# Optimization experiments

Hardware: AMD Instinct MI355X
Metric: run time of the kernel (lower is better)

The kernel has to match this reference:

```python
import jax, jax.numpy as jnp
import numpy as np

D_MODEL = 128
NUM_HEADS = 4
HEAD_DIM = D_MODEL // NUM_HEADS  # 32
SCALE = 1.0 / np.sqrt(HEAD_DIM)
LAMBDA_INIT = 0.8
EPS = 1e-5


def _layernorm(x, w, b):
    mu = jnp.mean(x, axis=-1, keepdims=True)
    var = jnp.var(x, axis=-1, keepdims=True)
    return (x - mu) * jax.lax.rsqrt(var + EPS) * w + b


def setup_inputs() -> dict:
    key = jax.random.key(0)
    ks = jax.random.split(key, 10)
    B, T, D = 8, 2048, D_MODEL
    inp = {
        "tokens": jax.random.normal(ks[0], (B, T, D), dtype=jnp.float32),
        "ln_w": jnp.ones((D,), jnp.float32),
        "ln_b": jnp.zeros((D,), jnp.float32),
        "wq": jax.random.normal(ks[1], (D, 2 * D), jnp.float32) * (1.0 / np.sqrt(D)),
        "wk": jax.random.normal(ks[2], (D, 2 * D), jnp.float32) * (1.0 / np.sqrt(D)),
        "wv": jax.random.normal(ks[3], (D, 2 * D), jnp.float32) * (1.0 / np.sqrt(D)),
        "wo": jax.random.normal(ks[4], (2 * D, D), jnp.float32) * (1.0 / np.sqrt(2 * D)),
        "lambda_q1": jax.random.normal(ks[5], (HEAD_DIM,), jnp.float32) * 0.1,
        "lambda_k1": jax.random.normal(ks[6], (HEAD_DIM,), jnp.float32) * 0.1,
        "lambda_q2": jax.random.normal(ks[7], (HEAD_DIM,), jnp.float32) * 0.1,
        "lambda_k2": jax.random.normal(ks[8], (HEAD_DIM,), jnp.float32) * 0.1,
        "sigma_signal": jnp.asarray(3.0, jnp.float32),
        "sigma_noise": jnp.asarray(10.0, jnp.float32),
        "hn_w": jnp.ones((2 * HEAD_DIM,), jnp.float32),
        "hn_b": jnp.zeros((2 * HEAD_DIM,), jnp.float32),
    }
    return inp


def reference(tokens, ln_w, ln_b, wq, wk, wv, wo,
              lambda_q1, lambda_k1, lambda_q2, lambda_k2,
              sigma_signal, sigma_noise, hn_w, hn_b):
    B, T, D = tokens.shape
    H, hd = NUM_HEADS, HEAD_DIM

    x = _layernorm(tokens, ln_w, ln_b)

    def heads(x, w):  # [B,T,D] @ [D,2D] -> [B,H,T,2*hd]
        return (x @ w).reshape(B, T, H, 2 * hd).transpose(0, 2, 1, 3)

    q = heads(x, wq)
    k = heads(x, wk)
    v = heads(x, wv)
    q1, q2 = q[..., :hd], q[..., hd:]
    k1, k2 = k[..., :hd], k[..., hd:]

    scores1 = jnp.einsum('bhqd,bhkd->bhqk', q1, k1) * SCALE
    scores2 = jnp.einsum('bhqd,bhkd->bhqk', q2, k2) * SCALE

    # temporal Gaussian bias, shared sigma mode: [T,T] broadcast over [B,H]
    pos = jnp.arange(T, dtype=tokens.dtype)
    rel = pos[None, :] - pos[:, None]  # rel_dist[i,j] = j - i
    sig_s = jnp.maximum(sigma_signal, 1.0)
    sig_n = jnp.maximum(sigma_noise, 1.0)
    scores1 = scores1 + (-0.5 * (rel / sig_s) ** 2)
    scores2 = scores2 + (-0.5 * (rel / sig_n) ** 2)

    attn1 = jax.nn.softmax(scores1, axis=-1)
    attn2 = jax.nn.softmax(scores2, axis=-1)

    lam = jnp.exp(jnp.dot(lambda_q1, lambda_k1)) - jnp.exp(jnp.dot(lambda_q2, lambda_k2)) + LAMBDA_INIT

    out = jnp.einsum('bhqk,bhkd->bhqd', attn1 - lam * attn2, v)  # [B,H,T,2*hd]
    out = _layernorm(out, hn_w, hn_b)
    out = out * (1.0 - LAMBDA_INIT)
    out = out.transpose(0, 2, 1, 3).reshape(B, T, 2 * D)
    out = out @ wo
    return tokens + out
```

## Files before the change

### kernel.cpp

```cpp
#include <hip/hip_runtime.h>
#include <hip/hip_bf16.h>

#define TSEQ 2048
#define BATCH 8
#define NHEAD 4
#define BH (BATCH*NHEAD)
#define HD 32
#define SCALE 0.17677669529663687f
#define L2E   1.4426950408889634f
#define SCALE2 (SCALE * L2E)
#define LAMBDA_INIT 0.8f
#define LN_EPS 1e-5f

#if __has_builtin(__builtin_amdgcn_exp2f)
#define EXP2F(x) __builtin_amdgcn_exp2f(x)
#else
#define EXP2F(x) __expf((x) * 0.6931471805599453f)
#endif

typedef __attribute__((ext_vector_type(8))) short short8;
typedef __attribute__((ext_vector_type(4))) float f32x4;

static __device__ __forceinline__ unsigned short f2bf(float x) {
    union { __hip_bfloat16 h; unsigned short u; } cv;
    cv.h = __float2bfloat16(x);
    return cv.u;
}

__global__ __launch_bounds__(256) void k_prep(
    const float* __restrict__ wq, const float* __restrict__ wk,
    const float* __restrict__ wv, const float* __restrict__ wo,
    const float* __restrict__ lq1, const float* __restrict__ lk1,
    const float* __restrict__ lq2, const float* __restrict__ lk2,
    const float* __restrict__ sig_s_p, const float* __restrict__ sig_n_p,
    unsigned short* __restrict__ WqkvT, unsigned short* __restrict__ WoT,
    float* __restrict__ scal)
{
    __shared__ float xt[64][65];
    const int bid = blockIdx.x, tid = threadIdx.x;

    if (bid == 0 && tid == 0) {
        float d1 = 0.f, d2 = 0.f;
        for (int i = 0; i < HD; i++) { d1 += lq1[i] * lk1[i]; d2 += lq2[i] * lk2[i]; }
        float lam = __expf(d1) - __expf(d2) + LAMBDA_INIT;
        float ss = fmaxf(sig_s_p[0], 1.f);
        float sn = fmaxf(sig_n_p[0], 1.f);
        int W = (int)ceilf(fmaxf(ss, sn) * 6.f);
        W = (W + 31) & ~31;
        if (W < 64) W = 64;
        scal[0] = lam;
        scal[1] = -0.5f / (ss * ss) * L2E;
        scal[2] = -0.5f / (sn * sn) * L2E;
        scal[3] = (float)W;
    }

    const float* src; int srcN, k0, nsrc0, dstK;
    unsigned short* dst;
    if (bid < 24) {
        int ntile = bid >> 1, ktile = bid & 1;
        int gn0 = ntile * 64; k0 = ktile * 64;
        int mat = gn0 >> 8;
        src = (mat == 0) ? wq : (mat == 1 ? wk : wv);
        srcN = 256; nsrc0 = gn0 & 255;
        dst = WqkvT + (size_t)gn0 * 128; dstK = 128;
    } else {
        int b2 = bid - 24;
        int ntile = b2 >> 2, ktile = b2 & 3;
        int gn0 = ntile * 64; k0 = ktile * 64;
        src = wo; srcN = 128; nsrc0 = gn0;
        dst = WoT + (size_t)gn0 * 256; dstK = 256;
    }
    {
        int r = tid >> 2, cs = tid & 3;
        const float* sp = src + (size_t)(k0 + r) * srcN + nsrc0 + cs * 16;
        #pragma unroll
        for (int j = 0; j < 4; j++) {
            float4 v = *(const float4*)(sp + j * 4);
            xt[r][cs * 16 + j * 4 + 0] = v.x;
            xt[r][cs * 16 + j * 4 + 1] = v.y;
            xt[r][cs * 16 + j * 4 + 2] = v.z;
            xt[r][cs * 16 + j * 4 + 3] = v.w;
        }
    }
    __syncthreads();
    {
        int n = tid >> 2, ks = tid & 3;
        short8 o0, o1;
        #pragma unroll
        for (int j = 0; j < 8; j++) {
            o0[j] = (short)f2bf(xt[ks * 16 + j][n]);
            o1[j] = (short)f2bf(xt[ks * 16 + 8 + j][n]);
        }
        unsigned short* dp = dst + (size_t)n * dstK + k0 + ks * 16;
        *(short8*)dp = o0;
        *(short8*)(dp + 8) = o1;
    }
}

__global__ __launch_bounds__(256) void k_qkv(
    const float* __restrict__ tokens, const float* __restrict__ ln_w,
    const float* __restrict__ ln_b, const unsigned short* __restrict__ WqkvT,
    unsigned short* __restrict__ Qg, unsigned short* __restrict__ Kg,
    unsigned short* __restrict__ Vtg)
{
    __shared__ unsigned short x_lds[32][132];
    __shared__ unsigned short c_lds[4][16][68];
    const int tid = threadIdx.x;
    const int r0 = blockIdx.x * 32;

    {
        int row = tid >> 3, sub = tid & 7;
        const float* tr = tokens + (size_t)(r0 + row) * 128 + sub * 16;
        float v[16]; float s = 0.f, sq = 0.f;
        #pragma unroll
        for (int j = 0; j < 16; j += 4) {
            float4 t4 = *(const float4*)(tr + j);
            v[j] = t4.x; v[j + 1] = t4.y; v[j + 2] = t4.z; v[j + 3] = t4.w;
        }
        #pragma unroll
        for (int j = 0; j < 16; j++) { s += v[j]; sq += v[j] * v[j]; }
        #pragma unroll
        for (int m = 1; m < 8; m <<= 1) { s += __shfl_xor(s, m, 64); sq += __shfl_xor(sq, m, 64); }
        float mean = s * (1.f / 128.f);
        float var  = sq * (1.f / 128.f) - mean * mean;
        float rstd = rsqrtf(var + LN_EPS);
        short8 o0, o1;
        #pragma unroll
        for (int j = 0; j < 8; j++) {
            int c0 = sub * 16 + j, c1 = sub * 16 + 8 + j;
            o0[j] = (short)f2bf((v[j] - mean) * rstd * ln_w[c0] + ln_b[c0]);
            o1[j] = (short)f2bf((v[8 + j] - mean) * rstd * ln_w[c1] + ln_b[c1]);
        }
        *(short8*)&x_lds[row][sub * 16] = o0;
        *(short8*)&x_lds[row][sub * 16 + 8] = o1;
    }
    __syncthreads();

    const int w = tid >> 6, lane = tid & 63;
    const int lg = lane >> 4, li = lane & 15;
    const int rt = w >> 1, ch = w & 1;

    short8 a[4];
    #pragma unroll
    for (int kc = 0; kc < 4; kc++)
        a[kc] = *(const short8*)&x_lds[rt * 16 + li][kc * 32 + lg * 8];

    const int b   = r0 >> 11;
    const int tw0 = (r0 & 2047) + rt * 16;

    #pragma unroll
    for (int cc = 0; cc < 6; cc++) {
        f32x4 acc[4] = {};
        #pragma unroll
        for (int t = 0; t < 4; t++) {
            int n0 = ch * 384 + cc * 64 + t * 16;
            const unsigned short* bp = WqkvT + (size_t)(n0 + li) * 128 + lg * 8;
            #pragma unroll
            for (int kc = 0; kc < 4; kc++) {
                short8 bf = *(const short8*)(bp + kc * 32);
                acc[t] = __builtin_amdgcn_mfma_f32_16x16x32_bf16(a[kc], bf, acc[t], 0, 0, 0);
            }
        }
        #pragma unroll
        for (int t = 0; t < 4; t++)
            #pragma unroll
            for (int r = 0; r < 4; r++)
                c_lds[w][lg * 4 + r][t * 16 + li] = f2bf(acc[t][r]);

        int gc = ch * 6 + cc;
        int kind = gc >> 2, h = gc & 3;
        size_t bhh = (size_t)(b * NHEAD + h);
        if (kind < 2) {
            unsigned short* base = (kind == 0) ? Qg : Kg;
            int row = lane >> 2, seg = lane & 3;
            unsigned short* dp = base + (bhh * TSEQ + tw0 + row) * 64 + seg * 16;
            *(short8*)dp       = *(const short8*)&c_lds[w][row][seg * 16];
            *(short8*)(dp + 8) = *(const short8*)&c_lds[w][row][seg * 16 + 8];
        } else {
            int d = lane;
            short8 v0, v1;
            #pragma unroll
            for (int j = 0; j < 8; j++) {
                v0[j] = (short)c_lds[w][j][d];
                v1[j] = (short)c_lds[w][8 + j][d];
            }
            unsigned short* dp = Vtg + (bhh * 64 + d) * TSEQ + tw0;
            *(short8*)dp = v0;
            *(short8*)(dp + 8) = v1;
        }
    }
}

__global__ __launch_bounds__(256) void k_attn2(
    const unsigned short* __restrict__ Qg, const unsigned short* __restrict__ Kg,
    const unsigned short* __restrict__ Vtg,
    const float* __restrict__ scal,
    const float* __restrict__ hn_w, const float* __restrict__ hn_b,
    const unsigned short* __restrict__ WoT, const float* __restrict__ tokens,
    float* __restrict__ out)
{
    __shared__ unsigned short p_lds[4][2][32][36];
    __shared__ unsigned short ao[32][264];

    const int tid  = threadIdx.x;
    const int w    = tid >> 6;
    const int lane = tid & 63;
    const int lg   = lane >> 4;
    const int li   = lane & 15;

    const int b  = blockIdx.x & 7;
    const int qw = (blockIdx.x >> 3) * 32;
    const int bh = b * NHEAD + w;

    const float lam = scal[0];
    const float c1  = scal[1];
    const float c2  = scal[2];
    const int   W   = (int)scal[3];

    int lo = qw - W; if (lo < 0) lo = 0; lo &= ~31;
    int hi = qw + 32 + W; hi = (hi + 31) & ~31; if (hi > TSEQ) hi = TSEQ;

    short8 q1[2], q2[2];
    #pragma unroll
    for (int qt = 0; qt < 2; qt++) {
        const unsigned short* qp = Qg + ((size_t)bh * TSEQ + (qw + qt * 16 + li)) * 64;
        q1[qt] = *(const short8*)(qp + lg * 8);
        q2[qt] = *(const short8*)(qp + 32 + lg * 8);
    }

    const unsigned short* kbase = Kg  + ((size_t)bh * TSEQ + li) * 64 + lg * 8;
    const unsigned short* vbase = Vtg + ((size_t)bh * 64 + li) * TSEQ + lg * 8;

    f32x4 acc1[2][4] = {}, acc2[2][4] = {};
    float ls1[2][4] = {}, ls2[2][4] = {};
    const f32x4 zero4 = {0.f, 0.f, 0.f, 0.f};

    short8 kf1c[2], kf2c[2];
    {
        const unsigned short* kp = kbase + (size_t)lo * 64;
        kf1c[0] = *(const short8*)(kp);
        kf2c[0] = *(const short8*)(kp + 32);
        kf1c[1] = *(const short8*)(kp + 1024);
        kf2c[1] = *(const short8*)(kp + 1024 + 32);
    }

    for (int kv = lo; kv < hi; kv += 32) {
        const unsigned short* vp = vbase + kv;
        short8 vf[4];
        #pragma unroll
        for (int dt = 0; dt < 4; dt++)
            vf[dt] = *(const short8*)(vp + (size_t)dt * 16 * TSEQ);

        short8 kf1n[2], kf2n[2];
        if (kv + 32 < hi) {
            const unsigned short* kp = kbase + (size_t)(kv + 32) * 64;
            kf1n[0] = *(const short8*)(kp);
            kf2n[0] = *(const short8*)(kp + 32);
            kf1n[1] = *(const short8*)(kp + 1024);
            kf2n[1] = *(const short8*)(kp + 1024 + 32);
        }

        #pragma unroll
        for (int qt = 0; qt < 2; qt++) {
            f32x4 s1[2], s2[2];
            #pragma unroll
            for (int kt = 0; kt < 2; kt++) {
                s1[kt] = __builtin_amdgcn_mfma_f32_16x16x32_bf16(q1[qt], kf1c[kt], zero4, 0, 0, 0);
                s2[kt] = __builtin_amdgcn_mfma_f32_16x16x32_bf16(q2[qt], kf2c[kt], zero4, 0, 0, 0);
            }
            const float rb = (float)(kv + li - qw - qt * 16 - 4 * lg);
            #pragma unroll
            for (int kt = 0; kt < 2; kt++) {
                #pragma unroll
                for (int r = 0; r < 4; r++) {
                    float rel = rb + (float)(16 * kt - r);
                    float rr  = rel * rel;
                    float e1  = EXP2F(fmaf(s1[kt][r], SCALE2, c1 * rr));
                    float e2  = EXP2F(fmaf(s2[kt][r], SCALE2, c2 * rr));
                    ls1[qt][r] += e1;
                    ls2[qt][r] += e2;
                    p_lds[w][0][qt * 16 + lg * 4 + r][kt * 16 + li] = f2bf(e1);
                    p_lds[w][1][qt * 16 + lg * 4 + r][kt * 16 + li] = f2bf(e2);
                }
            }
        }

        #pragma unroll
        for (int qt = 0; qt < 2; qt++) {
            short8 pa1 = *(const short8*)&p_lds[w][0][qt * 16 + li][lg * 8];
            short8 pa2 = *(const short8*)&p_lds[w][1][qt * 16 + li][lg * 8];
            #pragma unroll
            for (int dt = 0; dt < 4; dt++) {
                acc1[qt][dt] = __builtin_amdgcn_mfma_f32_16x16x32_bf16(pa1, vf[dt], acc1[qt][dt], 0, 0, 0);
                acc2[qt][dt] = __builtin_amdgcn_mfma_f32_16x16x32_bf16(pa2, vf[dt], acc2[qt][dt], 0, 0, 0);
            }
        }

        kf1c[0] = kf1n[0]; kf1c[1] = kf1n[1];
        kf2c[0] = kf2n[0]; kf2c[1] = kf2n[1];
    }

    #pragma unroll
    for (int qt = 0; qt < 2; qt++)
        #pragma unroll
        for (int r = 0; r < 4; r++) {
            #pragma unroll
            for (int m = 1; m < 16; m <<= 1) {
                ls1[qt][r] += __shfl_xor(ls1[qt][r], m, 64);
                ls2[qt][r] += __shfl_xor(ls2[qt][r], m, 64);
            }
        }

    {
        float hw[4], hb[4];
        #pragma unroll
        for (int t = 0; t < 4; t++) { hw[t] = hn_w[t * 16 + li]; hb[t] = hn_b[t * 16 + li]; }

        #pragma unroll
        for (int qt = 0; qt < 2; qt++) {
            #pragma unroll
            for (int r = 0; r < 4; r++) {
                float il1 = 1.f / ls1[qt][r];
                float il2 = lam / ls2[qt][r];
                float o[4];
                float s = 0.f, sq = 0.f;
                #pragma unroll
                for (int t = 0; t < 4; t++) {
                    o[t] = acc1[qt][t][r] * il1 - acc2[qt][t][r] * il2;
                    s += o[t]; sq += o[t] * o[t];
                }
                #pragma unroll
                for (int m = 1; m < 16; m <<= 1) { s += __shfl_xor(s, m, 64); sq += __shfl_xor(sq, m, 64); }
                float mean = s * (1.f / 64.f);
                float var  = sq * (1.f / 64.f) - mean * mean;
                float rstd = rsqrtf(var + LN_EPS);
                int arow = qt * 16 + lg * 4 + r;
                #pragma unroll
                for (int t = 0; t < 4; t++) {
                    ao[arow][w * 64 + t * 16 + li] =
                        f2bf(((o[t] - mean) * rstd * hw[t] + hb[t]) * 0.2f);
                }
            }
        }
    }
    __syncthreads();

    const int row0 = b * TSEQ + qw;
    #pragma unroll
    for (int c2 = 0; c2 < 2; c2++) {
        const int ct = w * 2 + c2;
        short8 bfr[8];
        const unsigned short* bp = WoT + (size_t)(ct * 16 + li) * 256 + lg * 8;
        #pragma unroll
        for (int kc = 0; kc < 8; kc++) bfr[kc] = *(const short8*)(bp + kc * 32);

        #pragma unroll
        for (int qt = 0; qt < 2; qt++) {
            f32x4 acc = {};
            #pragma unroll
            for (int kc = 0; kc < 8; kc++) {
                short8 af = *(const short8*)&ao[qt * 16 + li][kc * 32 + lg * 8];
                acc = __builtin_amdgcn_mfma_f32_16x16x32_bf16(af, bfr[kc], acc, 0, 0, 0);
            }
            #pragma unroll
            for (int r = 0; r < 4; r++) {
                size_t idx = (size_t)(row0 + qt * 16 + lg * 4 + r) * 128 + ct * 16 + li;
                out[idx] = tokens[idx] + acc[r];
            }
        }
    }
}

extern "C" void kernel_launch(void* const* d_in, const int* in_sizes, int n_in,
                              void* d_out, int out_size, void* d_ws, size_t ws_size,
                              hipStream_t stream) {
    const float* tokens = (const float*)d_in[0];
    const float* ln_w   = (const float*)d_in[1];
    const float* ln_b   = (const float*)d_in[2];
    const float* wq     = (const float*)d_in[3];
    const float* wk     = (const float*)d_in[4];
    const float* wv     = (const float*)d_in[5];
    const float* wo     = (const float*)d_in[6];
    const float* lq1    = (const float*)d_in[7];
    const float* lk1    = (const float*)d_in[8];
    const float* lq2    = (const float*)d_in[9];
    const float* lk2    = (const float*)d_in[10];
    const float* sigs   = (const float*)d_in[11];
    const float* sign   = (const float*)d_in[12];
    const float* hn_w   = (const float*)d_in[13];
    const float* hn_b   = (const float*)d_in[14];

    const size_t n_qk = (size_t)BH * TSEQ * 64;
    unsigned short* Qg      = (unsigned short*)d_ws;
    unsigned short* Kg      = Qg + n_qk;
    unsigned short* Vtg     = Kg + n_qk;
    unsigned short* WqkvT   = Vtg + n_qk;
    unsigned short* WoT     = WqkvT + 768 * 128;
    float*          scal    = (float*)(WoT + 128 * 256);

    k_prep<<<dim3(32), dim3(256), 0, stream>>>(
        wq, wk, wv, wo, lq1, lk1, lq2, lk2, sigs, sign, WqkvT, WoT, scal);
    k_qkv<<<dim3(BATCH * TSEQ / 32), dim3(256), 0, stream>>>(
        tokens, ln_w, ln_b, WqkvT, Qg, Kg, Vtg);
    k_attn2<<<dim3(512), dim3(256), 0, stream>>>(
        Qg, Kg, Vtg, scal, hn_w, hn_b, WoT, tokens, (float*)d_out);
}
```

Before: 60.97 us.

## Transpose MFMA operands to vectorize P stores and double-buffer KV tiles

Swaps the MFMA A/B operands in the QKV projection and the attention QK^T so each lane holds four consecutive columns. This lets Q/K be written directly to global memory with 4-wide stores and removes an LDS staging pass. In attention, P tiles are now written to LDS as packed 4-element vectors, and the row-sum reduction shrinks to two shuffles plus a broadcast. The KV loop now processes two 32-wide tiles per iteration with separate P buffers, and launch bounds request 2 blocks per CU, trading extra registers and LDS for more overlap.

```diff
diff --git a/kernel.cpp b/kernel.cpp
--- a/kernel.cpp
+++ b/kernel.cpp
@@ -19,6 +19,7 @@
 #endif
 
 typedef __attribute__((ext_vector_type(8))) short short8;
+typedef __attribute__((ext_vector_type(4))) short sv4;
 typedef __attribute__((ext_vector_type(4))) float f32x4;
 
 static __device__ __forceinline__ unsigned short f2bf(float x) {
@@ -104,7 +105,7 @@
     unsigned short* __restrict__ Vtg)
 {
     __shared__ unsigned short x_lds[32][132];
-    __shared__ unsigned short c_lds[4][16][68];
+    __shared__ unsigned short v_lds[4][64][18];
     const int tid = threadIdx.x;
     const int r0 = blockIdx.x * 32;
 
@@ -150,48 +151,48 @@
 
     #pragma unroll
     for (int cc = 0; cc < 6; cc++) {
+        const int gc = ch * 6 + cc;
+        const int kind = gc >> 2, h = gc & 3;
+        const size_t bhh = (size_t)(b * NHEAD + h);
+
         f32x4 acc[4] = {};
         #pragma unroll
         for (int t = 0; t < 4; t++) {
-            int n0 = ch * 384 + cc * 64 + t * 16;
+            int n0 = gc * 64 + t * 16;
             const unsigned short* bp = WqkvT + (size_t)(n0 + li) * 128 + lg * 8;
             #pragma unroll
             for (int kc = 0; kc < 4; kc++) {
                 short8 bf = *(const short8*)(bp + kc * 32);
-                acc[t] = __builtin_amdgcn_mfma_f32_16x16x32_bf16(a[kc], bf, acc[t], 0, 0, 0);
+                acc[t] = __builtin_amdgcn_mfma_f32_16x16x32_bf16(bf, a[kc], acc[t], 0, 0, 0);
             }
         }
-        #pragma unroll
-        for (int t = 0; t < 4; t++)
-            #pragma unroll
-            for (int r = 0; r < 4; r++)
-                c_lds[w][lg * 4 + r][t * 16 + li] = f2bf(acc[t][r]);
-
-        int gc = ch * 6 + cc;
-        int kind = gc >> 2, h = gc & 3;
-        size_t bhh = (size_t)(b * NHEAD + h);
+
         if (kind < 2) {
             unsigned short* base = (kind == 0) ? Qg : Kg;
-            int row = lane >> 2, seg = lane & 3;
-            unsigned short* dp = base + (bhh * TSEQ + tw0 + row) * 64 + seg * 16;
-            *(short8*)dp       = *(const short8*)&c_lds[w][row][seg * 16];
-            *(short8*)(dp + 8) = *(const short8*)&c_lds[w][row][seg * 16 + 8];
+            unsigned short* dp = base + (bhh * TSEQ + tw0 + li) * 64;
+            #pragma unroll
+            for (int t = 0; t < 4; t++) {
+                sv4 pk;
+                #pragma unroll
+                for (int r = 0; r < 4; r++) pk[r] = (short)f2bf(acc[t][r]);
+                *(sv4*)(dp + t * 16 + lg * 4) = pk;
+            }
         } else {
-            int d = lane;
-            short8 v0, v1;
-            #pragma unroll
-            for (int j = 0; j < 8; j++) {
-                v0[j] = (short)c_lds[w][j][d];
-                v1[j] = (short)c_lds[w][8 + j][d];
-            }
-            unsigned short* dp = Vtg + (bhh * 64 + d) * TSEQ + tw0;
+            #pragma unroll
+            for (int t = 0; t < 4; t++)
+                #pragma unroll
+                for (int r = 0; r < 4; r++)
+                    v_lds[w][t * 16 + lg * 4 + r][li] = f2bf(acc[t][r]);
+            short8 v0 = *(const short8*)&v_lds[w][lane][0];
+            short8 v1 = *(const short8*)&v_lds[w][lane][8];
+            unsigned short* dp = Vtg + (bhh * 64 + lane) * TSEQ + tw0;
             *(short8*)dp = v0;
             *(short8*)(dp + 8) = v1;
         }
     }
 }
 
-__global__ __launch_bounds__(256) void k_attn2(
+__global__ __launch_bounds__(256, 2) void k_attn2(
     const unsigned short* __restrict__ Qg, const unsigned short* __restrict__ Kg,
     const unsigned short* __restrict__ Vtg,
     const float* __restrict__ scal,
@@ -199,7 +200,8 @@
     const unsigned short* __restrict__ WoT, const float* __restrict__ tokens,
     float* __restrict__ out)
 {
-    __shared__ unsigned short p_lds[4][2][32][36];
+    __shared__ unsigned short pA_lds[4][2][32][36];
+    __shared__ unsigned short pB_lds[4][2][32][36];
     __shared__ unsigned short ao[32][264];
 
     const int tid  = threadIdx.x;
@@ -232,83 +234,101 @@
     const unsigned short* vbase = Vtg + ((size_t)bh * 64 + li) * TSEQ + lg * 8;
 
     f32x4 acc1[2][4] = {}, acc2[2][4] = {};
-    float ls1[2][4] = {}, ls2[2][4] = {};
+    float ls1[2] = {0.f, 0.f}, ls2[2] = {0.f, 0.f};
     const f32x4 zero4 = {0.f, 0.f, 0.f, 0.f};
 
-    short8 kf1c[2], kf2c[2];
-    {
-        const unsigned short* kp = kbase + (size_t)lo * 64;
-        kf1c[0] = *(const short8*)(kp);
-        kf2c[0] = *(const short8*)(kp + 32);
-        kf1c[1] = *(const short8*)(kp + 1024);
-        kf2c[1] = *(const short8*)(kp + 1024 + 32);
-    }
-
-    for (int kv = lo; kv < hi; kv += 32) {
-        const unsigned short* vp = vbase + kv;
-        short8 vf[4];
+#define QKEXP(KF1, KF2, KVB, PL)                                              \
+    {                                                                          \
+        _Pragma("unroll")                                                      \
+        for (int qt = 0; qt < 2; qt++) {                                       \
+            f32x4 s1[2], s2[2];                                                \
+            _Pragma("unroll")                                                  \
+            for (int kt = 0; kt < 2; kt++) {                                   \
+                s1[kt] = __builtin_amdgcn_mfma_f32_16x16x32_bf16(KF1[kt], q1[qt], zero4, 0, 0, 0); \
+                s2[kt] = __builtin_amdgcn_mfma_f32_16x16x32_bf16(KF2[kt], q2[qt], zero4, 0, 0, 0); \
+            }                                                                  \
+            const float rb = (float)((KVB) + lg * 4 - qw - qt * 16 - li);      \
+            _Pragma("unroll")                                                  \
+            for (int kt = 0; kt < 2; kt++) {                                   \
+                sv4 pk1, pk2;                                                  \
+                _Pragma("unroll")                                              \
+                for (int r = 0; r < 4; r++) {                                  \
+                    float rel = rb + (float)(16 * kt + r);                     \
+                    float rr  = rel * rel;                                     \
+                    float e1  = EXP2F(fmaf(s1[kt][r], SCALE2, c1 * rr));       \
+                    float e2  = EXP2F(fmaf(s2[kt][r], SCALE2, c2 * rr));       \
+                    ls1[qt] += e1; ls2[qt] += e2;                              \
+                    pk1[r] = (short)f2bf(e1); pk2[r] = (short)f2bf(e2);        \
+                }                                                              \
+                *(sv4*)&PL[w][0][qt * 16 + li][kt * 16 + lg * 4] = pk1;        \
+                *(sv4*)&PL[w][1][qt * 16 + li][kt * 16 + lg * 4] = pk2;        \
+            }                                                                  \
+        }                                                                      \
+    }
+
+#define PVACC(PL, VF)                                                          \
+    {                                                                          \
+        _Pragma("unroll")                                                      \
+        for (int qt = 0; qt < 2; qt++) {                                       \
+            short8 pa1 = *(const short8*)&PL[w][0][qt * 16 + li][lg * 8];      \
+            short8 pa2 = *(const short8*)&PL[w][1][qt * 16 + li][lg * 8];      \
+            _Pragma("unroll")                                                  \
+            for (int dt = 0; dt < 4; dt++) {                                   \
+                acc1[qt][dt] = __builtin_amdgcn_mfma_f32_16x16x32_bf16(pa1, VF[dt], acc1[qt][dt], 0, 0, 0); \
+                acc2[qt][dt] = __builtin_amdgcn_mfma_f32_16x16x32_bf16(pa2, VF[dt], acc2[qt][dt], 0, 0, 0); \
+            }                                                                  \
+        }                                                                      \
+    }
+
+    for (int kv = lo; kv < hi; kv += 64) {
+        const bool two = (kv + 32) < hi;
+
+        const unsigned short* kpA = kbase + (size_t)kv * 64;
+        short8 ka1[2], ka2[2], va[4];
+        ka1[0] = *(const short8*)(kpA);
+        ka2[0] = *(const short8*)(kpA + 32);
+        ka1[1] = *(const short8*)(kpA + 1024);
+        ka2[1] = *(const short8*)(kpA + 1024 + 32);
+        const unsigned short* vpA = vbase + kv;
         #pragma unroll
         for (int dt = 0; dt < 4; dt++)
-            vf[dt] = *(const short8*)(vp + (size_t)dt * 16 * TSEQ);
-
-        short8 kf1n[2], kf2n[2];
-        if (kv + 32 < hi) {
-            const unsigned short* kp = kbase + (size_t)(kv + 32) * 64;
-            kf1n[0] = *(const short8*)(kp);
-            kf2n[0] = *(const short8*)(kp + 32);
-            kf1n[1] = *(const short8*)(kp + 1024);
-            kf2n[1] = *(const short8*)(kp + 1024 + 32);
-        }
-
-        #pragma unroll
-        for (int qt = 0; qt < 2; qt++) {
-            f32x4 s1[2], s2[2];
-            #pragma unroll
-            for (int kt = 0; kt < 2; kt++) {
-                s1[kt] = __builtin_amdgcn_mfma_f32_16x16x32_bf16(q1[qt], kf1c[kt], zero4, 0, 0, 0);
-                s2[kt] = __builtin_amdgcn_mfma_f32_16x16x32_bf16(q2[qt], kf2c[kt], zero4, 0, 0, 0);
-            }
-            const float rb = (float)(kv + li - qw - qt * 16 - 4 * lg);
-            #pragma unroll
-            for (int kt = 0; kt < 2; kt++) {
-                #pragma unroll
-                for (int r = 0; r < 4; r++) {
-                    float rel = rb + (float)(16 * kt - r);
-                    float rr  = rel * rel;
-                    float e1  = EXP2F(fmaf(s1[kt][r], SCALE2, c1 * rr));
-                    float e2  = EXP2F(fmaf(s2[kt][r], SCALE2, c2 * rr));
-                    ls1[qt][r] += e1;
-                    ls2[qt][r] += e2;
-                    p_lds[w][0][qt * 16 + lg * 4 + r][kt * 16 + li] = f2bf(e1);
-                    p_lds[w][1][qt * 16 + lg * 4 + r][kt * 16 + li] = f2bf(e2);
-                }
-            }
-        }
-
-        #pragma unroll
-        for (int qt = 0; qt < 2; qt++) {
-            short8 pa1 = *(const short8*)&p_lds[w][0][qt * 16 + li][lg * 8];
-            short8 pa2 = *(const short8*)&p_lds[w][1][qt * 16 + li][lg * 8];
-            #pragma unroll
-            for (int dt = 0; dt < 4; dt++) {
-                acc1[qt][dt] = __builtin_amdgcn_mfma_f32_16x16x32_bf16(pa1, vf[dt], acc1[qt][dt], 0, 0, 0);
-                acc2[qt][dt] = __builtin_amdgcn_mfma_f32_16x16x32_bf16(pa2, vf[dt], acc2[qt][dt], 0, 0, 0);
-            }
-        }
-
-        kf1c[0] = kf1n[0]; kf1c[1] = kf1n[1];
-        kf2c[0] = kf2n[0]; kf2c[1] = kf2n[1];
-    }
-
+            va[dt] = *(const short8*)(vpA + (size_t)dt * 16 * TSEQ);
+
+        short8 kb1[2], kb2[2], vb[4];
+        if (two) {
+            const unsigned short* kpB = kbase + (size_t)(kv + 32) * 64;
+            kb1[0] = *(const short8*)(kpB);
+            kb2[0] = *(const short8*)(kpB + 32);
+            kb1[1] = *(const short8*)(kpB + 1024);
+            kb2[1] = *(const short8*)(kpB + 1024 + 32);
+            const unsigned short* vpB = vbase + kv + 32;
+            #pragma unroll
+            for (int dt = 0; dt < 4; dt++)
+                vb[dt] = *(const short8*)(vpB + (size_t)dt * 16 * TSEQ);
+        }
+
+        QKEXP(ka1, ka2, kv, pA_lds)
+        if (two) QKEXP(kb1, kb2, kv + 32, pB_lds)
+        PVACC(pA_lds, va)
+        if (two) PVACC(pB_lds, vb)
+    }
+#undef QKEXP
+#undef PVACC
+
+    #pragma unroll
+    for (int qt = 0; qt < 2; qt++) {
+        ls1[qt] += __shfl_xor(ls1[qt], 16, 64);
+        ls1[qt] += __shfl_xor(ls1[qt], 32, 64);
+        ls2[qt] += __shfl_xor(ls2[qt], 16, 64);
+        ls2[qt] += __shfl_xor(ls2[qt], 32, 64);
+    }
+    float l1q[2][4], l2q[2][4];
     #pragma unroll
     for (int qt = 0; qt < 2; qt++)
         #pragma unroll
         for (int r = 0; r < 4; r++) {
-            #pragma unroll
-            for (int m = 1; m < 16; m <<= 1) {
-                ls1[qt][r] += __shfl_xor(ls1[qt][r], m, 64);
-                ls2[qt][r] += __shfl_xor(ls2[qt][r], m, 64);
-            }
+            l1q[qt][r] = __shfl(ls1[qt], lg * 4 + r, 64);
+            l2q[qt][r] = __shfl(ls2[qt], lg * 4 + r, 64);
         }
 
     {
@@ -320,8 +340,8 @@
         for (int qt = 0; qt < 2; qt++) {
             #pragma unroll
             for (int r = 0; r < 4; r++) {
-                float il1 = 1.f / ls1[qt][r];
-                float il2 = lam / ls2[qt][r];
+                float il1 = 1.f / l1q[qt][r];
+                float il2 = lam / l2q[qt][r];
                 float o[4];
                 float s = 0.f, sq = 0.f;
                 #pragma unroll
```

New measurement: 61.96 us. Within noise of the previous version (+1.6%).

## Split attention KV range across two wave groups with LDS reduction

Applied to the files above, without the earlier changes.

Doubles the attention block to 512 threads. Each head gets two waves, and each wave processes half of the banded KV tile range. The partial accumulators and row sums from the second group are reduced into the first group through shared memory reused from the P buffer, in two phases separated by barriers. The output projection now assigns one column tile per wave. The aim is more waves in flight across the 512 blocks to hide latency, at the cost of extra barriers, LDS traffic and tighter register limits.

```diff
diff --git a/kernel.cpp b/kernel.cpp
--- a/kernel.cpp
+++ b/kernel.cpp
@@ -191,7 +191,7 @@
     }
 }
 
-__global__ __launch_bounds__(256) void k_attn2(
+__global__ __launch_bounds__(512, 4) void k_attn2(
     const unsigned short* __restrict__ Qg, const unsigned short* __restrict__ Kg,
     const unsigned short* __restrict__ Vtg,
     const float* __restrict__ scal,
@@ -199,18 +199,24 @@
     const unsigned short* __restrict__ WoT, const float* __restrict__ tokens,
     float* __restrict__ out)
 {
-    __shared__ unsigned short p_lds[4][2][32][36];
+    __shared__ __align__(16) char smem_u[41984];
+    typedef unsigned short plds_t[2][32][36];
+    plds_t* p_lds = (plds_t*)smem_u;
+    typedef f32x4 red_t[20][64];
+    red_t* red = (red_t*)smem_u;
     __shared__ unsigned short ao[32][264];
 
     const int tid  = threadIdx.x;
     const int w    = tid >> 6;
+    const int h    = w & 3;
+    const int g    = w >> 2;
     const int lane = tid & 63;
     const int lg   = lane >> 4;
     const int li   = lane & 15;
 
     const int b  = blockIdx.x & 7;
     const int qw = (blockIdx.x >> 3) * 32;
-    const int bh = b * NHEAD + w;
+    const int bh = b * NHEAD + h;
 
     const float lam = scal[0];
     const float c1  = scal[1];
@@ -219,6 +225,11 @@
 
     int lo = qw - W; if (lo < 0) lo = 0; lo &= ~31;
     int hi = qw + 32 + W; hi = (hi + 31) & ~31; if (hi > TSEQ) hi = TSEQ;
+
+    const int nt   = (hi - lo) >> 5;
+    const int ntA  = (nt + 1) >> 1;
+    const int myLo = g ? (lo + (ntA << 5)) : lo;
+    const int myHi = g ? hi : (lo + (ntA << 5));
 
     short8 q1[2], q2[2];
     #pragma unroll
@@ -232,19 +243,19 @@
     const unsigned short* vbase = Vtg + ((size_t)bh * 64 + li) * TSEQ + lg * 8;
 
     f32x4 acc1[2][4] = {}, acc2[2][4] = {};
-    float ls1[2][4] = {}, ls2[2][4] = {};
+    f32x4 lsv1[2] = {}, lsv2[2] = {};
     const f32x4 zero4 = {0.f, 0.f, 0.f, 0.f};
 
     short8 kf1c[2], kf2c[2];
-    {
-        const unsigned short* kp = kbase + (size_t)lo * 64;
+    if (myLo < myHi) {
+        const unsigned short* kp = kbase + (size_t)myLo * 64;
         kf1c[0] = *(const short8*)(kp);
         kf2c[0] = *(const short8*)(kp + 32);
         kf1c[1] = *(const short8*)(kp + 1024);
         kf2c[1] = *(const short8*)(kp + 1024 + 32);
     }
 
-    for (int kv = lo; kv < hi; kv += 32) {
+    for (int kv = myLo; kv < myHi; kv += 32) {
         const unsigned short* vp = vbase + kv;
         short8 vf[4];
         #pragma unroll
@@ -252,7 +263,7 @@
             vf[dt] = *(const short8*)(vp + (size_t)dt * 16 * TSEQ);
 
         short8 kf1n[2], kf2n[2];
-        if (kv + 32 < hi) {
+        if (kv + 32 < myHi) {
             const unsigned short* kp = kbase + (size_t)(kv + 32) * 64;
             kf1n[0] = *(const short8*)(kp);
             kf2n[0] = *(const short8*)(kp + 32);
@@ -277,8 +288,8 @@
                     float rr  = rel * rel;
                     float e1  = EXP2F(fmaf(s1[kt][r], SCALE2, c1 * rr));
                     float e2  = EXP2F(fmaf(s2[kt][r], SCALE2, c2 * rr));
-                    ls1[qt][r] += e1;
-                    ls2[qt][r] += e2;
+                    lsv1[qt][r] += e1;
+                    lsv2[qt][r] += e2;
                     p_lds[w][0][qt * 16 + lg * 4 + r][kt * 16 + li] = f2bf(e1);
                     p_lds[w][1][qt * 16 + lg * 4 + r][kt * 16 + li] = f2bf(e2);
                 }
@@ -300,18 +311,56 @@
         kf2c[0] = kf2n[0]; kf2c[1] = kf2n[1];
     }
 
-    #pragma unroll
-    for (int qt = 0; qt < 2; qt++)
-        #pragma unroll
-        for (int r = 0; r < 4; r++) {
-            #pragma unroll
-            for (int m = 1; m < 16; m <<= 1) {
-                ls1[qt][r] += __shfl_xor(ls1[qt][r], m, 64);
-                ls2[qt][r] += __shfl_xor(ls2[qt][r], m, 64);
-            }
-        }
-
-    {
+#define WRITE_RED(HH)                                                         \
+    {                                                                          \
+        _Pragma("unroll")                                                      \
+        for (int qt = 0; qt < 2; qt++)                                         \
+            _Pragma("unroll")                                                  \
+            for (int dt = 0; dt < 4; dt++) {                                   \
+                red[HH][qt * 4 + dt][lane] = acc1[qt][dt];                     \
+                red[HH][8 + qt * 4 + dt][lane] = acc2[qt][dt];                 \
+            }                                                                  \
+        red[HH][16][lane] = lsv1[0]; red[HH][17][lane] = lsv1[1];              \
+        red[HH][18][lane] = lsv2[0]; red[HH][19][lane] = lsv2[1];              \
+    }
+#define ADD_RED(HH)                                                           \
+    {                                                                          \
+        _Pragma("unroll")                                                      \
+        for (int qt = 0; qt < 2; qt++)                                         \
+            _Pragma("unroll")                                                  \
+            for (int dt = 0; dt < 4; dt++) {                                   \
+                acc1[qt][dt] += red[HH][qt * 4 + dt][lane];                    \
+                acc2[qt][dt] += red[HH][8 + qt * 4 + dt][lane];                \
+            }                                                                  \
+        lsv1[0] += red[HH][16][lane]; lsv1[1] += red[HH][17][lane];            \
+        lsv2[0] += red[HH][18][lane]; lsv2[1] += red[HH][19][lane];            \
+    }
+
+    const int hh = h & 1;
+    const bool p0 = (h >> 1) == 0;
+    __syncthreads();
+    if (g == 1 && p0) WRITE_RED(hh)
+    __syncthreads();
+    if (g == 0 && p0) ADD_RED(hh)
+    __syncthreads();
+    if (g == 1 && !p0) WRITE_RED(hh)
+    __syncthreads();
+    if (g == 0 && !p0) ADD_RED(hh)
+#undef WRITE_RED
+#undef ADD_RED
+
+    if (g == 0) {
+        #pragma unroll
+        for (int qt = 0; qt < 2; qt++)
+            #pragma unroll
+            for (int r = 0; r < 4; r++) {
+                #pragma unroll
+                for (int m = 1; m < 16; m <<= 1) {
+                    lsv1[qt][r] += __shfl_xor(lsv1[qt][r], m, 64);
+                    lsv2[qt][r] += __shfl_xor(lsv2[qt][r], m, 64);
+                }
+            }
+
         float hw[4], hb[4];
         #pragma unroll
         for (int t = 0; t < 4; t++) { hw[t] = hn_w[t * 16 + li]; hb[t] = hn_b[t * 16 + li]; }
@@ -320,8 +369,8 @@
         for (int qt = 0; qt < 2; qt++) {
             #pragma unroll
             for (int r = 0; r < 4; r++) {
-                float il1 = 1.f / ls1[qt][r];
-                float il2 = lam / ls2[qt][r];
+                float il1 = 1.f / lsv1[qt][r];
+                float il2 = lam / lsv2[qt][r];
                 float o[4];
                 float s = 0.f, sq = 0.f;
                 #pragma unroll
@@ -337,7 +386,7 @@
                 int arow = qt * 16 + lg * 4 + r;
                 #pragma unroll
                 for (int t = 0; t < 4; t++) {
-                    ao[arow][w * 64 + t * 16 + li] =
+                    ao[arow][h * 64 + t * 16 + li] =
                         f2bf(((o[t] - mean) * rstd * hw[t] + hb[t]) * 0.2f);
                 }
             }
@@ -346,9 +395,8 @@
     __syncthreads();
 
     const int row0 = b * TSEQ + qw;
-    #pragma unroll
-    for (int c2 = 0; c2 < 2; c2++) {
-        const int ct = w * 2 + c2;
+    {
+        const int ct = w;
         short8 bfr[8];
         const unsigned short* bp = WoT + (size_t)(ct * 16 + li) * 256 + lg * 8;
         #pragma unroll
@@ -402,6 +450,6 @@
         wq, wk, wv, wo, lq1, lk1, lq2, lk2, sigs, sign, WqkvT, WoT, scal);
     k_qkv<<<dim3(BATCH * TSEQ / 32), dim3(256), 0, stream>>>(
         tokens, ln_w, ln_b, WqkvT, Qg, Kg, Vtg);
-    k_attn2<<<dim3(512), dim3(256), 0, stream>>>(
+    k_attn2<<<dim3(512), dim3(512), 0, stream>>>(
         Qg, Kg, Vtg, scal, hn_w, hn_b, WoT, tokens, (float*)d_out);
 }
```

Result: slower. 104.2 us (+71.0%).
